# Optimization experiments

Measured on AMD Instinct MI355X. Metric: run time of the kernel, lower is better.

## Reference

```python
import jax, jax.numpy as jnp
import numpy as np
import math

D_K = 64

def setup_inputs() -> dict:
    key = jax.random.key(0)
    k1, k2, k3, k4 = jax.random.split(key, 4)
    BH, S, dk = 32, 2048, D_K
    q = jax.random.normal(k1, (BH, S, dk), dtype=jnp.float32)
    k = jax.random.normal(k2, (BH, S, dk), dtype=jnp.float32)
    v = jax.random.normal(k3, (BH, S, dk), dtype=jnp.float32)
    mask = jax.random.uniform(k4, (BH, S, S), dtype=jnp.float32)
    return {"q": q, "k": k, "v": v, "mask": mask}

def reference(q, k, v, mask):
    # scores: [BH, S, S]
    scores = jnp.einsum('bqd,bkd->bqk', q, k) * (1.0 / math.sqrt(D_K))
    masked = scores * mask  # multiplicative mask before softmax
    attn = jax.nn.softmax(masked, axis=-1)
    return jnp.einsum('bqk,bkd->bqd', attn, v)
```

## Files before the change

kernel.cpp:

```cpp
#include <hip/hip_runtime.h>
#include <hip/hip_bf16.h>

#define BH    32
#define SEQ   2048
#define DK    64
#define QBLK  256
#define KBLK  64
#define NIT   (SEQ / KBLK)
#define KSTR  72

typedef short  short8  __attribute__((ext_vector_type(8)));
typedef float  f32x4   __attribute__((ext_vector_type(4)));
typedef float  float4v __attribute__((ext_vector_type(4)));
typedef unsigned short ushort4v __attribute__((ext_vector_type(4)));

__device__ __forceinline__ unsigned short f2bf(float f) {
    unsigned int u = __builtin_bit_cast(unsigned int, f);
    u += 0x7FFFu + ((u >> 16) & 1u);
    return (unsigned short)(u >> 16);
}

#if __has_builtin(__builtin_amdgcn_exp2f)
#define EXP2F(x) __builtin_amdgcn_exp2f(x)
#else
#define EXP2F(x) exp2f(x)
#endif

__global__ __launch_bounds__(1024, 4)
void sdpa_kernel(const float* __restrict__ Q, const float* __restrict__ K,
                 const float* __restrict__ V, const float* __restrict__ M,
                 float* __restrict__ O)
{
    __shared__ unsigned short sK [KBLK][KSTR];
    __shared__ unsigned short sVt[DK][KSTR];
    __shared__ unsigned short sP [16][16][KSTR];

    const int tid  = threadIdx.x;
    const int wave = tid >> 6;
    const int lane = tid & 63;
    const int g    = lane >> 4;
    const int li   = lane & 15;

    const int b  = blockIdx.x;
    const int qb = blockIdx.y * QBLK;

    const float* Kb = K + (size_t)b * SEQ * DK;
    const float* Vb = V + (size_t)b * SEQ * DK;

    const float QSC = 0.125f * 1.44269504f;
    short8 aq[2];
    {
        const size_t qoff = ((size_t)b * SEQ + (qb + wave * 16 + li)) * DK;
        #pragma unroll
        for (int kk = 0; kk < 2; ++kk) {
            const float* qp = Q + qoff + kk * 32 + g * 8;
            float4v q0 = *(const float4v*)(qp);
            float4v q1 = *(const float4v*)(qp + 4);
            #pragma unroll
            for (int i = 0; i < 4; ++i) {
                aq[kk][i]     = (short)f2bf(q0[i] * QSC);
                aq[kk][i + 4] = (short)f2bf(q1[i] * QSC);
            }
        }
    }

    const int sr = tid >> 4;
    const int sc = (tid & 15) * 4;
    const int vd = tid & 63;
    const int vk = (tid >> 6) * 4;

    const float* kp = Kb + (size_t)sr * DK + sc;
    const float* vp = Vb + (size_t)vk * DK + vd;
    const float* mbase = M + ((size_t)b * SEQ + (qb + wave * 16 + g * 4)) * SEQ + li;

    float4v kreg = *(const float4v*)kp;
    float vreg0 = vp[0 * DK], vreg1 = vp[1 * DK], vreg2 = vp[2 * DK], vreg3 = vp[3 * DK];

    f32x4 oacc[4] = {};
    float lsum[4] = {0.f, 0.f, 0.f, 0.f};

    for (int it = 0; it < NIT; ++it) {
        __syncthreads();
        {
            ushort4v pk;
            pk[0] = f2bf(kreg[0]); pk[1] = f2bf(kreg[1]);
            pk[2] = f2bf(kreg[2]); pk[3] = f2bf(kreg[3]);
            *(ushort4v*)(&sK[sr][sc]) = pk;
            ushort4v pv_;
            pv_[0] = f2bf(vreg0); pv_[1] = f2bf(vreg1);
            pv_[2] = f2bf(vreg2); pv_[3] = f2bf(vreg3);
            *(ushort4v*)(&sVt[vd][vk]) = pv_;
        }
        __syncthreads();

        float mk[4][4];
        {
            const float* mp = mbase + (size_t)it * KBLK;
            #pragma unroll
            for (int r = 0; r < 4; ++r)
                #pragma unroll
                for (int t = 0; t < 4; ++t)
                    mk[r][t] = mp[(size_t)r * SEQ + t * 16];
        }

        if (it + 1 < NIT) {
            kp += KBLK * DK;  vp += KBLK * DK;
            kreg = *(const float4v*)kp;
            vreg0 = vp[0 * DK]; vreg1 = vp[1 * DK];
            vreg2 = vp[2 * DK]; vreg3 = vp[3 * DK];
        }

        f32x4 sacc[4] = {};
        #pragma unroll
        for (int t = 0; t < 4; ++t) {
            #pragma unroll
            for (int kk = 0; kk < 2; ++kk) {
                short8 bk = *(const short8*)(&sK[t * 16 + li][kk * 32 + g * 8]);
                sacc[t] = __builtin_amdgcn_mfma_f32_16x16x32_bf16(aq[kk], bk, sacc[t], 0, 0, 0);
            }
        }

        #pragma unroll
        for (int r = 0; r < 4; ++r) {
            float p0 = EXP2F(sacc[0][r] * mk[r][0]);
            float p1 = EXP2F(sacc[1][r] * mk[r][1]);
            float p2 = EXP2F(sacc[2][r] * mk[r][2]);
            float p3 = EXP2F(sacc[3][r] * mk[r][3]);
            lsum[r] += (p0 + p1) + (p2 + p3);
            sP[wave][g * 4 + r][0 * 16 + li] = f2bf(p0);
            sP[wave][g * 4 + r][1 * 16 + li] = f2bf(p1);
            sP[wave][g * 4 + r][2 * 16 + li] = f2bf(p2);
            sP[wave][g * 4 + r][3 * 16 + li] = f2bf(p3);
        }

        #pragma unroll
        for (int kk = 0; kk < 2; ++kk) {
            short8 pa = *(const short8*)(&sP[wave][li][kk * 32 + g * 8]);
            #pragma unroll
            for (int dt = 0; dt < 4; ++dt) {
                short8 bv = *(const short8*)(&sVt[dt * 16 + li][kk * 32 + g * 8]);
                oacc[dt] = __builtin_amdgcn_mfma_f32_16x16x32_bf16(pa, bv, oacc[dt], 0, 0, 0);
            }
        }
    }

    #pragma unroll
    for (int r = 0; r < 4; ++r) {
        float l = lsum[r];
        l += __shfl_xor(l, 1);
        l += __shfl_xor(l, 2);
        l += __shfl_xor(l, 4);
        l += __shfl_xor(l, 8);
        float inv = 1.0f / l;
        size_t orow = ((size_t)b * SEQ + (qb + wave * 16 + g * 4 + r)) * DK;
        #pragma unroll
        for (int dt = 0; dt < 4; ++dt)
            O[orow + dt * 16 + li] = oacc[dt][r] * inv;
    }
}

extern "C" void kernel_launch(void* const* d_in, const int* in_sizes, int n_in,
                              void* d_out, int out_size, void* d_ws, size_t ws_size,
                              hipStream_t stream) {
    const float* q = (const float*)d_in[0];
    const float* k = (const float*)d_in[1];
    const float* v = (const float*)d_in[2];
    const float* m = (const float*)d_in[3];
    float* o = (float*)d_out;

    dim3 grid(BH, SEQ / QBLK);
    sdpa_kernel<<<grid, dim3(1024), 0, stream>>>(q, k, v, m, o);
}
```

Before: 146.1 us.

## Double-buffer K/V shared tiles and halve query block to 512 threads

The K and V^T shared-memory tiles are now double-buffered, so the next tile's bf16 conversion and store overlap with compute on the current buffer. This cuts the two barriers per iteration down to one. The query block shrinks from 256 to 128 rows with 512 threads per block, which doubles the grid and makes each thread stage more K/V elements. K/V reuse per block falls and global K/V traffic doubles, in exchange for more blocks and fewer syncs.

```diff
diff --git a/kernel.cpp b/kernel.cpp
--- a/kernel.cpp
+++ b/kernel.cpp
@@ -4,7 +4,7 @@
 #define BH    32
 #define SEQ   2048
 #define DK    64
-#define QBLK  256
+#define QBLK  128
 #define KBLK  64
 #define NIT   (SEQ / KBLK)
 #define KSTR  72
@@ -13,6 +13,7 @@
 typedef float  f32x4   __attribute__((ext_vector_type(4)));
 typedef float  float4v __attribute__((ext_vector_type(4)));
 typedef unsigned short ushort4v __attribute__((ext_vector_type(4)));
+typedef unsigned short ushort8v __attribute__((ext_vector_type(8)));
 
 __device__ __forceinline__ unsigned short f2bf(float f) {
     unsigned int u = __builtin_bit_cast(unsigned int, f);
@@ -26,14 +27,14 @@
 #define EXP2F(x) exp2f(x)
 #endif
 
-__global__ __launch_bounds__(1024, 4)
+__global__ __launch_bounds__(512, 4)
 void sdpa_kernel(const float* __restrict__ Q, const float* __restrict__ K,
                  const float* __restrict__ V, const float* __restrict__ M,
                  float* __restrict__ O)
 {
-    __shared__ unsigned short sK [KBLK][KSTR];
-    __shared__ unsigned short sVt[DK][KSTR];
-    __shared__ unsigned short sP [16][16][KSTR];
+    __shared__ unsigned short sK [2][KBLK][KSTR];
+    __shared__ unsigned short sVt[2][DK][KSTR];
+    __shared__ unsigned short sP [8][16][KSTR];
 
     const int tid  = threadIdx.x;
     const int wave = tid >> 6;
@@ -67,31 +68,44 @@
     const int sr = tid >> 4;
     const int sc = (tid & 15) * 4;
     const int vd = tid & 63;
-    const int vk = (tid >> 6) * 4;
+    const int vk = (tid >> 6) * 8;
 
     const float* kp = Kb + (size_t)sr * DK + sc;
     const float* vp = Vb + (size_t)vk * DK + vd;
     const float* mbase = M + ((size_t)b * SEQ + (qb + wave * 16 + g * 4)) * SEQ + li;
 
-    float4v kreg = *(const float4v*)kp;
-    float vreg0 = vp[0 * DK], vreg1 = vp[1 * DK], vreg2 = vp[2 * DK], vreg3 = vp[3 * DK];
+    float4v kr0, kr1;
+    float vr[8];
+
+    kr0 = *(const float4v*)(kp);
+    kr1 = *(const float4v*)(kp + 32 * DK);
+    #pragma unroll
+    for (int j = 0; j < 8; ++j) vr[j] = vp[j * DK];
+
+    {
+        ushort4v pk0, pk1;
+        #pragma unroll
+        for (int e = 0; e < 4; ++e) { pk0[e] = f2bf(kr0[e]); pk1[e] = f2bf(kr1[e]); }
+        *(ushort4v*)(&sK[0][sr][sc])      = pk0;
+        *(ushort4v*)(&sK[0][sr + 32][sc]) = pk1;
+        ushort8v pv_;
+        #pragma unroll
+        for (int e = 0; e < 8; ++e) pv_[e] = f2bf(vr[e]);
+        *(ushort8v*)(&sVt[0][vd][vk]) = pv_;
+    }
+    kp += KBLK * DK;  vp += KBLK * DK;
+    kr0 = *(const float4v*)(kp);
+    kr1 = *(const float4v*)(kp + 32 * DK);
+    #pragma unroll
+    for (int j = 0; j < 8; ++j) vr[j] = vp[j * DK];
+
+    __syncthreads();
 
     f32x4 oacc[4] = {};
     float lsum[4] = {0.f, 0.f, 0.f, 0.f};
 
     for (int it = 0; it < NIT; ++it) {
-        __syncthreads();
-        {
-            ushort4v pk;
-            pk[0] = f2bf(kreg[0]); pk[1] = f2bf(kreg[1]);
-            pk[2] = f2bf(kreg[2]); pk[3] = f2bf(kreg[3]);
-            *(ushort4v*)(&sK[sr][sc]) = pk;
-            ushort4v pv_;
-            pv_[0] = f2bf(vreg0); pv_[1] = f2bf(vreg1);
-            pv_[2] = f2bf(vreg2); pv_[3] = f2bf(vreg3);
-            *(ushort4v*)(&sVt[vd][vk]) = pv_;
-        }
-        __syncthreads();
+        const int cb = it & 1;
 
         float mk[4][4];
         {
@@ -104,10 +118,24 @@
         }
 
         if (it + 1 < NIT) {
-            kp += KBLK * DK;  vp += KBLK * DK;
-            kreg = *(const float4v*)kp;
-            vreg0 = vp[0 * DK]; vreg1 = vp[1 * DK];
-            vreg2 = vp[2 * DK]; vreg3 = vp[3 * DK];
+            const int nb = cb ^ 1;
+            ushort4v pk0, pk1;
+            #pragma unroll
+            for (int e = 0; e < 4; ++e) { pk0[e] = f2bf(kr0[e]); pk1[e] = f2bf(kr1[e]); }
+            *(ushort4v*)(&sK[nb][sr][sc])      = pk0;
+            *(ushort4v*)(&sK[nb][sr + 32][sc]) = pk1;
+            ushort8v pv_;
+            #pragma unroll
+            for (int e = 0; e < 8; ++e) pv_[e] = f2bf(vr[e]);
+            *(ushort8v*)(&sVt[nb][vd][vk]) = pv_;
+
+            if (it + 2 < NIT) {
+                kp += KBLK * DK;  vp += KBLK * DK;
+                kr0 = *(const float4v*)(kp);
+                kr1 = *(const float4v*)(kp + 32 * DK);
+                #pragma unroll
+                for (int j = 0; j < 8; ++j) vr[j] = vp[j * DK];
+            }
         }
 
         f32x4 sacc[4] = {};
@@ -115,7 +143,7 @@
         for (int t = 0; t < 4; ++t) {
             #pragma unroll
             for (int kk = 0; kk < 2; ++kk) {
-                short8 bk = *(const short8*)(&sK[t * 16 + li][kk * 32 + g * 8]);
+                short8 bk = *(const short8*)(&sK[cb][t * 16 + li][kk * 32 + g * 8]);
                 sacc[t] = __builtin_amdgcn_mfma_f32_16x16x32_bf16(aq[kk], bk, sacc[t], 0, 0, 0);
             }
         }
@@ -138,10 +166,12 @@
             short8 pa = *(const short8*)(&sP[wave][li][kk * 32 + g * 8]);
             #pragma unroll
             for (int dt = 0; dt < 4; ++dt) {
-                short8 bv = *(const short8*)(&sVt[dt * 16 + li][kk * 32 + g * 8]);
+                short8 bv = *(const short8*)(&sVt[cb][dt * 16 + li][kk * 32 + g * 8]);
                 oacc[dt] = __builtin_amdgcn_mfma_f32_16x16x32_bf16(pa, bv, oacc[dt], 0, 0, 0);
             }
         }
+
+        __syncthreads();
     }
 
     #pragma unroll
@@ -169,5 +199,5 @@
     float* o = (float*)d_out;
 
     dim3 grid(BH, SEQ / QBLK);
-    sdpa_kernel<<<grid, dim3(1024), 0, stream>>>(q, k, v, m, o);
+    sdpa_kernel<<<grid, dim3(512), 0, stream>>>(q, k, v, m, o);
 }
```

Measured after the change: 174.8 us. +19.6%, slower.

## Pre-pack K and V to bf16 (V transposed) in workspace before attention

Applied to the files above, without the earlier changes.

Adds a pre-pass kernel that converts K to bf16 and V to transposed bf16 in the workspace. The attention kernel then loads bf16 tiles straight into shared memory, with no per-iteration fp32-to-bf16 conversion and no strided V loads. Each of the 8 query blocks per head no longer redundantly reads and converts the fp32 K and V. The cost is an extra launch and a round trip through global memory for the packed data. It falls back to the old fp32 kernel when the workspace is too small.

```diff
diff --git a/kernel.cpp b/kernel.cpp
--- a/kernel.cpp
+++ b/kernel.cpp
@@ -13,6 +13,7 @@
 typedef float  f32x4   __attribute__((ext_vector_type(4)));
 typedef float  float4v __attribute__((ext_vector_type(4)));
 typedef unsigned short ushort4v __attribute__((ext_vector_type(4)));
+typedef unsigned short ushort8v __attribute__((ext_vector_type(8)));
 
 __device__ __forceinline__ unsigned short f2bf(float f) {
     unsigned int u = __builtin_bit_cast(unsigned int, f);
@@ -26,10 +27,183 @@
 #define EXP2F(x) exp2f(x)
 #endif
 
+__global__ __launch_bounds__(256)
+void pack_kv(const float* __restrict__ K, const float* __restrict__ V,
+             unsigned short* __restrict__ Kbf, unsigned short* __restrict__ Vt)
+{
+    __shared__ unsigned short tl[DK][KSTR];
+    const int b   = blockIdx.x;
+    const int kb  = blockIdx.y * KBLK;
+    const int tid = threadIdx.x;
+    const int r   = tid >> 2;
+    const int c   = (tid & 3) * 16;
+
+    {
+        const float* src = K + ((size_t)b * SEQ + kb + r) * DK + c;
+        float4v a0 = *(const float4v*)(src);
+        float4v a1 = *(const float4v*)(src + 4);
+        float4v a2 = *(const float4v*)(src + 8);
+        float4v a3 = *(const float4v*)(src + 12);
+        ushort8v o0, o1;
+        #pragma unroll
+        for (int e = 0; e < 4; ++e) {
+            o0[e] = f2bf(a0[e]); o0[e + 4] = f2bf(a1[e]);
+            o1[e] = f2bf(a2[e]); o1[e + 4] = f2bf(a3[e]);
+        }
+        unsigned short* dst = Kbf + ((size_t)b * SEQ + kb + r) * DK + c;
+        *(ushort8v*)(dst)     = o0;
+        *(ushort8v*)(dst + 8) = o1;
+    }
+    {
+        const float* src = V + ((size_t)b * SEQ + kb + r) * DK + c;
+        float4v a0 = *(const float4v*)(src);
+        float4v a1 = *(const float4v*)(src + 4);
+        float4v a2 = *(const float4v*)(src + 8);
+        float4v a3 = *(const float4v*)(src + 12);
+        #pragma unroll
+        for (int e = 0; e < 4; ++e) {
+            tl[c + e     ][r] = f2bf(a0[e]);
+            tl[c + e + 4 ][r] = f2bf(a1[e]);
+            tl[c + e + 8 ][r] = f2bf(a2[e]);
+            tl[c + e + 12][r] = f2bf(a3[e]);
+        }
+    }
+    __syncthreads();
+    {
+        const int d  = tid >> 2;
+        const int ch = (tid & 3) * 16;
+        ushort8v w0 = *(const ushort8v*)(&tl[d][ch]);
+        ushort8v w1 = *(const ushort8v*)(&tl[d][ch + 8]);
+        unsigned short* dst = Vt + ((size_t)b * DK + d) * SEQ + kb + ch;
+        *(ushort8v*)(dst)     = w0;
+        *(ushort8v*)(dst + 8) = w1;
+    }
+}
+
 __global__ __launch_bounds__(1024, 4)
-void sdpa_kernel(const float* __restrict__ Q, const float* __restrict__ K,
-                 const float* __restrict__ V, const float* __restrict__ M,
-                 float* __restrict__ O)
+void sdpa_bf16(const float* __restrict__ Q, const unsigned short* __restrict__ Kbf,
+               const unsigned short* __restrict__ Vt, const float* __restrict__ M,
+               float* __restrict__ O)
+{
+    __shared__ unsigned short sK [KBLK][KSTR];
+    __shared__ unsigned short sVt[DK][KSTR];
+    __shared__ unsigned short sP [16][16][KSTR];
+
+    const int tid  = threadIdx.x;
+    const int wave = tid >> 6;
+    const int lane = tid & 63;
+    const int g    = lane >> 4;
+    const int li   = lane & 15;
+
+    const int b  = blockIdx.x;
+    const int qb = blockIdx.y * QBLK;
+
+    const float QSC = 0.125f * 1.44269504f;
+    short8 aq[2];
+    {
+        const size_t qoff = ((size_t)b * SEQ + (qb + wave * 16 + li)) * DK;
+        #pragma unroll
+        for (int kk = 0; kk < 2; ++kk) {
+            const float* qp = Q + qoff + kk * 32 + g * 8;
+            float4v q0 = *(const float4v*)(qp);
+            float4v q1 = *(const float4v*)(qp + 4);
+            #pragma unroll
+            for (int i = 0; i < 4; ++i) {
+                aq[kk][i]     = (short)f2bf(q0[i] * QSC);
+                aq[kk][i + 4] = (short)f2bf(q1[i] * QSC);
+            }
+        }
+    }
+
+    const int sr = tid >> 4;
+    const int sc = (tid & 15) * 4;
+
+    const unsigned short* kp = Kbf + (size_t)b * SEQ * DK + (size_t)sr * DK + sc;
+    const unsigned short* vp = Vt  + (size_t)b * DK * SEQ + (size_t)sr * SEQ + sc;
+    const float* mbase = M + ((size_t)b * SEQ + (qb + wave * 16 + g * 4)) * SEQ + li;
+
+    ushort4v kreg = *(const ushort4v*)kp;
+    ushort4v vreg = *(const ushort4v*)vp;
+
+    f32x4 oacc[4] = {};
+    float lsum[4] = {0.f, 0.f, 0.f, 0.f};
+
+    for (int it = 0; it < NIT; ++it) {
+        __syncthreads();
+        *(ushort4v*)(&sK [sr][sc]) = kreg;
+        *(ushort4v*)(&sVt[sr][sc]) = vreg;
+        __syncthreads();
+
+        float mk[4][4];
+        {
+            const float* mp = mbase + (size_t)it * KBLK;
+            #pragma unroll
+            for (int r = 0; r < 4; ++r)
+                #pragma unroll
+                for (int t = 0; t < 4; ++t)
+                    mk[r][t] = mp[(size_t)r * SEQ + t * 16];
+        }
+
+        if (it + 1 < NIT) {
+            kp += KBLK * DK;
+            vp += KBLK;
+            kreg = *(const ushort4v*)kp;
+            vreg = *(const ushort4v*)vp;
+        }
+
+        f32x4 sacc[4] = {};
+        #pragma unroll
+        for (int t = 0; t < 4; ++t) {
+            #pragma unroll
+            for (int kk = 0; kk < 2; ++kk) {
+                short8 bk = *(const short8*)(&sK[t * 16 + li][kk * 32 + g * 8]);
+                sacc[t] = __builtin_amdgcn_mfma_f32_16x16x32_bf16(aq[kk], bk, sacc[t], 0, 0, 0);
+            }
+        }
+
+        #pragma unroll
+        for (int r = 0; r < 4; ++r) {
+            float p0 = EXP2F(sacc[0][r] * mk[r][0]);
+            float p1 = EXP2F(sacc[1][r] * mk[r][1]);
+            float p2 = EXP2F(sacc[2][r] * mk[r][2]);
+            float p3 = EXP2F(sacc[3][r] * mk[r][3]);
+            lsum[r] += (p0 + p1) + (p2 + p3);
+            sP[wave][g * 4 + r][0 * 16 + li] = f2bf(p0);
+            sP[wave][g * 4 + r][1 * 16 + li] = f2bf(p1);
+            sP[wave][g * 4 + r][2 * 16 + li] = f2bf(p2);
+            sP[wave][g * 4 + r][3 * 16 + li] = f2bf(p3);
+        }
+
+        #pragma unroll
+        for (int kk = 0; kk < 2; ++kk) {
+            short8 pa = *(const short8*)(&sP[wave][li][kk * 32 + g * 8]);
+            #pragma unroll
+            for (int dt = 0; dt < 4; ++dt) {
+                short8 bv = *(const short8*)(&sVt[dt * 16 + li][kk * 32 + g * 8]);
+                oacc[dt] = __builtin_amdgcn_mfma_f32_16x16x32_bf16(pa, bv, oacc[dt], 0, 0, 0);
+            }
+        }
+    }
+
+    #pragma unroll
+    for (int r = 0; r < 4; ++r) {
+        float l = lsum[r];
+        l += __shfl_xor(l, 1);
+        l += __shfl_xor(l, 2);
+        l += __shfl_xor(l, 4);
+        l += __shfl_xor(l, 8);
+        float inv = 1.0f / l;
+        size_t orow = ((size_t)b * SEQ + (qb + wave * 16 + g * 4 + r)) * DK;
+        #pragma unroll
+        for (int dt = 0; dt < 4; ++dt)
+            O[orow + dt * 16 + li] = oacc[dt][r] * inv;
+    }
+}
+
+__global__ __launch_bounds__(1024, 4)
+void sdpa_f32(const float* __restrict__ Q, const float* __restrict__ K,
+              const float* __restrict__ V, const float* __restrict__ M,
+              float* __restrict__ O)
 {
     __shared__ unsigned short sK [KBLK][KSTR];
     __shared__ unsigned short sVt[DK][KSTR];
@@ -168,6 +342,15 @@
     const float* m = (const float*)d_in[3];
     float* o = (float*)d_out;
 
-    dim3 grid(BH, SEQ / QBLK);
-    sdpa_kernel<<<grid, dim3(1024), 0, stream>>>(q, k, v, m, o);
-}
+    const size_t kv_elems = (size_t)BH * SEQ * DK;
+    const size_t need     = kv_elems * 2 * sizeof(unsigned short);
+
+    if (ws_size >= need) {
+        unsigned short* Kbf = (unsigned short*)d_ws;
+        unsigned short* Vt  = Kbf + kv_elems;
+        pack_kv<<<dim3(BH, SEQ / KBLK), dim3(256), 0, stream>>>(k, v, Kbf, Vt);
+        sdpa_bf16<<<dim3(BH, SEQ / QBLK), dim3(1024), 0, stream>>>(q, Kbf, Vt, m, o);
+    } else {
+        sdpa_f32<<<dim3(BH, SEQ / QBLK), dim3(1024), 0, stream>>>(q, k, v, m, o);
+    }
+}
```

Result: slower. 157.2 us (+7.5%).

## Double-buffer K/V shared tiles and prefetch mask one iteration ahead

Applied to the files above, without the earlier changes.

K and V shared-memory tiles are now double-buffered, so the next tile is converted and stored while the current one is consumed. This cuts the loop from two barriers per iteration to one. Mask values are also loaded one iteration ahead into ping-pong register arrays, with the loop manually unrolled by two, to hide global-load latency for the mask. The cost is extra LDS and register pressure with 1024-thread blocks, which could lower occupancy.

```diff
diff --git a/kernel.cpp b/kernel.cpp
--- a/kernel.cpp
+++ b/kernel.cpp
@@ -31,8 +31,8 @@
                  const float* __restrict__ V, const float* __restrict__ M,
                  float* __restrict__ O)
 {
-    __shared__ unsigned short sK [KBLK][KSTR];
-    __shared__ unsigned short sVt[DK][KSTR];
+    __shared__ unsigned short sK [2][KBLK][KSTR];
+    __shared__ unsigned short sVt[2][DK][KSTR];
     __shared__ unsigned short sP [16][16][KSTR];
 
     const int tid  = threadIdx.x;
@@ -75,74 +75,96 @@
 
     float4v kreg = *(const float4v*)kp;
     float vreg0 = vp[0 * DK], vreg1 = vp[1 * DK], vreg2 = vp[2 * DK], vreg3 = vp[3 * DK];
+    {
+        ushort4v pk;
+        pk[0] = f2bf(kreg[0]); pk[1] = f2bf(kreg[1]);
+        pk[2] = f2bf(kreg[2]); pk[3] = f2bf(kreg[3]);
+        *(ushort4v*)(&sK[0][sr][sc]) = pk;
+        ushort4v pv_;
+        pv_[0] = f2bf(vreg0); pv_[1] = f2bf(vreg1);
+        pv_[2] = f2bf(vreg2); pv_[3] = f2bf(vreg3);
+        *(ushort4v*)(&sVt[0][vd][vk]) = pv_;
+    }
+    kp += KBLK * DK;  vp += KBLK * DK;
+    kreg = *(const float4v*)kp;
+    vreg0 = vp[0 * DK]; vreg1 = vp[1 * DK]; vreg2 = vp[2 * DK]; vreg3 = vp[3 * DK];
+
+    float mkA[4][4], mkB[4][4];
+    #pragma unroll
+    for (int r = 0; r < 4; ++r) {
+        #pragma unroll
+        for (int t = 0; t < 4; ++t)
+            mkA[r][t] = mbase[(size_t)r * SEQ + t * 16];
+    }
+
+    __syncthreads();
 
     f32x4 oacc[4] = {};
     float lsum[4] = {0.f, 0.f, 0.f, 0.f};
 
-    for (int it = 0; it < NIT; ++it) {
-        __syncthreads();
-        {
-            ushort4v pk;
-            pk[0] = f2bf(kreg[0]); pk[1] = f2bf(kreg[1]);
-            pk[2] = f2bf(kreg[2]); pk[3] = f2bf(kreg[3]);
-            *(ushort4v*)(&sK[sr][sc]) = pk;
-            ushort4v pv_;
-            pv_[0] = f2bf(vreg0); pv_[1] = f2bf(vreg1);
-            pv_[2] = f2bf(vreg2); pv_[3] = f2bf(vreg3);
-            *(ushort4v*)(&sVt[vd][vk]) = pv_;
-        }
-        __syncthreads();
+#define SDPA_BODY(IT, CUR, MKC, MKN)                                          \
+    {                                                                         \
+        if ((IT) + 1 < NIT) {                                                 \
+            const float* mp = mbase + (size_t)((IT) + 1) * KBLK;              \
+            _Pragma("unroll")                                                 \
+            for (int r = 0; r < 4; ++r) {                                     \
+                _Pragma("unroll")                                             \
+                for (int t = 0; t < 4; ++t)                                   \
+                    MKN[r][t] = mp[(size_t)r * SEQ + t * 16];                 \
+            }                                                                 \
+            ushort4v pk;                                                      \
+            pk[0] = f2bf(kreg[0]); pk[1] = f2bf(kreg[1]);                     \
+            pk[2] = f2bf(kreg[2]); pk[3] = f2bf(kreg[3]);                     \
+            *(ushort4v*)(&sK[(CUR) ^ 1][sr][sc]) = pk;                        \
+            ushort4v pv_;                                                     \
+            pv_[0] = f2bf(vreg0); pv_[1] = f2bf(vreg1);                       \
+            pv_[2] = f2bf(vreg2); pv_[3] = f2bf(vreg3);                       \
+            *(ushort4v*)(&sVt[(CUR) ^ 1][vd][vk]) = pv_;                      \
+            if ((IT) + 2 < NIT) {                                             \
+                kp += KBLK * DK;  vp += KBLK * DK;                            \
+                kreg = *(const float4v*)kp;                                   \
+                vreg0 = vp[0 * DK]; vreg1 = vp[1 * DK];                       \
+                vreg2 = vp[2 * DK]; vreg3 = vp[3 * DK];                       \
+            }                                                                 \
+        }                                                                     \
+        f32x4 sacc[4] = {};                                                   \
+        _Pragma("unroll")                                                     \
+        for (int t = 0; t < 4; ++t) {                                         \
+            _Pragma("unroll")                                                 \
+            for (int kk = 0; kk < 2; ++kk) {                                  \
+                short8 bk = *(const short8*)(&sK[CUR][t * 16 + li][kk * 32 + g * 8]); \
+                sacc[t] = __builtin_amdgcn_mfma_f32_16x16x32_bf16(aq[kk], bk, sacc[t], 0, 0, 0); \
+            }                                                                 \
+        }                                                                     \
+        _Pragma("unroll")                                                     \
+        for (int r = 0; r < 4; ++r) {                                         \
+            float p0 = EXP2F(sacc[0][r] * MKC[r][0]);                         \
+            float p1 = EXP2F(sacc[1][r] * MKC[r][1]);                         \
+            float p2 = EXP2F(sacc[2][r] * MKC[r][2]);                         \
+            float p3 = EXP2F(sacc[3][r] * MKC[r][3]);                         \
+            lsum[r] += (p0 + p1) + (p2 + p3);                                 \
+            sP[wave][g * 4 + r][0 * 16 + li] = f2bf(p0);                      \
+            sP[wave][g * 4 + r][1 * 16 + li] = f2bf(p1);                      \
+            sP[wave][g * 4 + r][2 * 16 + li] = f2bf(p2);                      \
+            sP[wave][g * 4 + r][3 * 16 + li] = f2bf(p3);                      \
+        }                                                                     \
+        _Pragma("unroll")                                                     \
+        for (int kk = 0; kk < 2; ++kk) {                                      \
+            short8 pa = *(const short8*)(&sP[wave][li][kk * 32 + g * 8]);     \
+            _Pragma("unroll")                                                 \
+            for (int dt = 0; dt < 4; ++dt) {                                  \
+                short8 bv = *(const short8*)(&sVt[CUR][dt * 16 + li][kk * 32 + g * 8]); \
+                oacc[dt] = __builtin_amdgcn_mfma_f32_16x16x32_bf16(pa, bv, oacc[dt], 0, 0, 0); \
+            }                                                                 \
+        }                                                                     \
+        __syncthreads();                                                      \
+    }
 
-        float mk[4][4];
-        {
-            const float* mp = mbase + (size_t)it * KBLK;
-            #pragma unroll
-            for (int r = 0; r < 4; ++r)
-                #pragma unroll
-                for (int t = 0; t < 4; ++t)
-                    mk[r][t] = mp[(size_t)r * SEQ + t * 16];
-        }
-
-        if (it + 1 < NIT) {
-            kp += KBLK * DK;  vp += KBLK * DK;
-            kreg = *(const float4v*)kp;
-            vreg0 = vp[0 * DK]; vreg1 = vp[1 * DK];
-            vreg2 = vp[2 * DK]; vreg3 = vp[3 * DK];
-        }
-
-        f32x4 sacc[4] = {};
-        #pragma unroll
-        for (int t = 0; t < 4; ++t) {
-            #pragma unroll
-            for (int kk = 0; kk < 2; ++kk) {
-                short8 bk = *(const short8*)(&sK[t * 16 + li][kk * 32 + g * 8]);
-                sacc[t] = __builtin_amdgcn_mfma_f32_16x16x32_bf16(aq[kk], bk, sacc[t], 0, 0, 0);
-            }
-        }
-
-        #pragma unroll
-        for (int r = 0; r < 4; ++r) {
-            float p0 = EXP2F(sacc[0][r] * mk[r][0]);
-            float p1 = EXP2F(sacc[1][r] * mk[r][1]);
-            float p2 = EXP2F(sacc[2][r] * mk[r][2]);
-            float p3 = EXP2F(sacc[3][r] * mk[r][3]);
-            lsum[r] += (p0 + p1) + (p2 + p3);
-            sP[wave][g * 4 + r][0 * 16 + li] = f2bf(p0);
-            sP[wave][g * 4 + r][1 * 16 + li] = f2bf(p1);
-            sP[wave][g * 4 + r][2 * 16 + li] = f2bf(p2);
-            sP[wave][g * 4 + r][3 * 16 + li] = f2bf(p3);
-        }
-
-        #pragma unroll
-        for (int kk = 0; kk < 2; ++kk) {
-            short8 pa = *(const short8*)(&sP[wave][li][kk * 32 + g * 8]);
-            #pragma unroll
-            for (int dt = 0; dt < 4; ++dt) {
-                short8 bv = *(const short8*)(&sVt[dt * 16 + li][kk * 32 + g * 8]);
-                oacc[dt] = __builtin_amdgcn_mfma_f32_16x16x32_bf16(pa, bv, oacc[dt], 0, 0, 0);
-            }
-        }
+    for (int it = 0; it < NIT; it += 2) {
+        SDPA_BODY(it,     0, mkA, mkB)
+        SDPA_BODY(it + 1, 1, mkB, mkA)
     }
+#undef SDPA_BODY
 
     #pragma unroll
     for (int r = 0; r < 4; ++r) {
```

After: 138.5 us, median of 2. 1.05x faster.
